# Performance work log

Measured on AMD Instinct MI355X. Metric: run time of the kernel, lower is better.

## Reference

```python
import jax, jax.numpy as jnp
import numpy as np

K = 7        # kernel_size (window)
PAD = 3      # padding = K // 2, stride = 1 -> spatial size preserved
G = 64       # groups
COUT = 64    # out_channels; d = COUT // G = 1 per-group channel dim
D = COUT // G


def _gconv(x, W):
    # grouped 1x1 conv: x [B, C, H, W], W [g, d_out_g, c_in_g] -> [B, g, d_out_g, H, W]
    B, C, H, Wd = x.shape
    g, d, c = W.shape
    return jnp.einsum('bgchw,gdc->bgdhw', x.reshape(B, g, c, H, Wd), W)


def _windows(x, k):
    # torch unfold(2,k,1).unfold(3,k,1) then flatten: row-major (i, j) window order
    # x [B, G, D, Hp, Wp] -> [B, G, D, H, W, k*k]
    Hp, Wp = x.shape[-2:]
    H, W = Hp - k + 1, Wp - k + 1
    return jnp.stack([x[..., i:i + H, j:j + W] for i in range(k) for j in range(k)], axis=-1)


def setup_inputs() -> dict:
    key = jax.random.key(0)
    ks = jax.random.split(key, 8)
    B, CIN, H, W = 4, 64, 56, 56
    RDIM = 256
    kaiming = np.sqrt(2.0 / COUT).astype(np.float32)  # fan_out for 1x1 conv
    x = jax.random.normal(ks[0], (B, CIN, H, W), jnp.float32)
    r = jax.random.normal(ks[1], (1, RDIM, K, K), jnp.float32)
    Wq = jax.random.normal(ks[2], (G, D, CIN // G), jnp.float32) * kaiming
    Wk = jax.random.normal(ks[3], (G, D, CIN // G), jnp.float32) * kaiming
    Wv = jax.random.normal(ks[4], (G, D, CIN // G), jnp.float32) * kaiming
    Wr = jax.random.normal(ks[5], (G, D, RDIM // G), jnp.float32) * kaiming
    u_p = jax.random.normal(ks[6], (1, G, D, 1, 1, 1), jnp.float32)
    v_p = jax.random.normal(ks[7], (1, G, D, 1, 1, 1), jnp.float32)
    return {'x': x, 'r': r, 'Wq': Wq, 'Wk': Wk, 'Wv': Wv, 'Wr': Wr, 'u_p': u_p, 'v_p': v_p}


def reference(x, r, Wq, Wk, Wv, Wr, u_p, v_p):
    B, _, H, W = x.shape
    xp = jnp.pad(x, ((0, 0), (0, 0), (PAD, PAD), (PAD, PAD)))
    q = _gconv(x, Wq)[..., None]              # [B,G,D,H,W,1]
    k_w = _windows(_gconv(xp, Wk), K)          # [B,G,D,H,W,K*K]
    v_w = _windows(_gconv(xp, Wv), K)          # [B,G,D,H,W,K*K]
    r_o = _gconv(r, Wr).reshape(1, G, D, 1, 1, K * K)
    # original: q*k + q*r + u*k + v*r == (q+u)*k + (q+v)*r
    # NOTE: original scale uses INTEGER division np.sqrt(groups // out_channels);
    # with groups == out_channels this is sqrt(1) = 1.0 (faithful).
    scale = float(np.sqrt(G // COUT))
    logits = ((q + u_p) * k_w + (q + v_p) * r_o).sum(axis=2, keepdims=True) * scale
    attn = jax.nn.softmax(logits, axis=-1)     # softmax over K*K window
    out = (attn * v_w).sum(axis=-1)            # [B,G,D,H,W]
    return out.reshape(B, -1, H, W)
```

## Files before the change

### kernel.cpp

```cpp
#include <hip/hip_runtime.h>
#include <hip/hip_bf16.h>

#define KW    7
#define PADW  3
#define HW    56
#define ROWS  8
#define TILE_H (ROWS + KW - 1)
#define TILE_W 64
#define NTHREADS 448
#define NCHUNK 7

#define LOG2E 1.44269504088896340736f

__global__ __launch_bounds__(NTHREADS) void saconv_kernel(
    const float* __restrict__ x,
    const float* __restrict__ r,
    const float* __restrict__ Wq,
    const float* __restrict__ Wk,
    const float* __restrict__ Wv,
    const float* __restrict__ Wr,
    const float* __restrict__ up,
    const float* __restrict__ vp,
    float* __restrict__ out)
{
    __shared__ float xs[TILE_H][TILE_W];
    __shared__ float ro[KW * KW];

    const int tid   = threadIdx.x;
    const int bid   = blockIdx.x;
    const int chunk = bid % NCHUNK;
    const int g     = (bid / NCHUNK) & 63;
    const int b     = bid / (NCHUNK * 64);
    const int y0    = chunk * ROWS;

    const float wq = Wq[g];
    const float wk = Wk[g];
    const float wv = Wv[g];
    const float ug = up[g];
    const float vg = vp[g];

    if (tid < KW * KW) {
        float acc = 0.f;
#pragma unroll
        for (int c = 0; c < 4; ++c) {
            acc += r[(g * 4 + c) * (KW * KW) + tid] * Wr[g * 4 + c];
        }
        ro[tid] = acc;
    }

    const float* xb = x + (size_t)(b * 64 + g) * (HW * HW);
    for (int idx = tid; idx < TILE_H * 62; idx += NTHREADS) {
        const int ty = idx / 62;
        const int tx = idx - ty * 62;
        const int gy = y0 - PADW + ty;
        const int gx = tx - PADW;
        float v = 0.f;
        if (gy >= 0 && gy < HW && gx >= 0 && gx < HW)
            v = xb[gy * HW + gx];
        xs[ty][tx] = v;
    }
    __syncthreads();

    const int row = tid / HW;
    const int col = tid - row * HW;

    const float xc  = xs[row + PADW][col + PADW];
    const float q   = xc * wq;
    const float a2  = (q + ug) * wk * LOG2E;
    const float cc2 = (q + vg) * LOG2E;

    float se = 0.f, sx = 0.f;
#pragma unroll
    for (int i = 0; i < KW; ++i) {
#pragma unroll
        for (int j = 0; j < KW; ++j) {
            const float xv = xs[row + i][col + j];
            const float l2 = __builtin_fmaf(a2, xv, cc2 * ro[i * KW + j]);
            const float e  = __builtin_amdgcn_exp2f(l2);
            se += e;
            sx = __builtin_fmaf(e, xv, sx);
        }
    }

    out[((size_t)(b * 64 + g) * HW + (y0 + row)) * HW + col] =
        wv * sx * __builtin_amdgcn_rcpf(se);
}

extern "C" void kernel_launch(void* const* d_in, const int* in_sizes, int n_in,
                              void* d_out, int out_size, void* d_ws, size_t ws_size,
                              hipStream_t stream) {
    const float* x  = (const float*)d_in[0];
    const float* r  = (const float*)d_in[1];
    const float* Wq = (const float*)d_in[2];
    const float* Wk = (const float*)d_in[3];
    const float* Wv = (const float*)d_in[4];
    const float* Wr = (const float*)d_in[5];
    const float* up = (const float*)d_in[6];
    const float* vp = (const float*)d_in[7];
    float* out = (float*)d_out;

    const int grid = 4 * 64 * NCHUNK;
    saconv_kernel<<<grid, NTHREADS, 0, stream>>>(x, r, Wq, Wk, Wv, Wr, up, vp, out);
}
```

Baseline: 76.43 us.

## Process two groups per block with float2 packed math and interleaved shared tile

Each block now handles a pair of groups. Shared memory holds an interleaved float2 tile and float2 relative logits, so the window loop can use packed FP32 ops (v_pk_fma/v_pk_mul) and 64-bit LDS reads. This halves the number of blocks, amortises the index math, and reduces LDS instructions per output. In exchange it doubles the LDS footprint per block and leaves fewer blocks to fill the GPU (896 vs 1792). The exp2 calls stay scalar.

```diff
diff --git a/kernel.cpp b/kernel.cpp
--- a/kernel.cpp
+++ b/kernel.cpp
@@ -12,6 +12,8 @@
 
 #define LOG2E 1.44269504088896340736f
 
+typedef float f2 __attribute__((ext_vector_type(2)));
+
 __global__ __launch_bounds__(NTHREADS) void saconv_kernel(
     const float* __restrict__ x,
     const float* __restrict__ r,
@@ -23,40 +25,47 @@
     const float* __restrict__ vp,
     float* __restrict__ out)
 {
-    __shared__ float xs[TILE_H][TILE_W];
-    __shared__ float ro[KW * KW];
+    __shared__ f2 xs[TILE_H][TILE_W];
+    __shared__ f2 ro2[KW * KW];
 
     const int tid   = threadIdx.x;
     const int bid   = blockIdx.x;
     const int chunk = bid % NCHUNK;
-    const int g     = (bid / NCHUNK) & 63;
-    const int b     = bid / (NCHUNK * 64);
+    const int gp    = (bid / NCHUNK) & 31;
+    const int b     = bid / (NCHUNK * 32);
     const int y0    = chunk * ROWS;
+    const int g0    = 2 * gp;
+    const int g1    = 2 * gp + 1;
 
-    const float wq = Wq[g];
-    const float wk = Wk[g];
-    const float wv = Wv[g];
-    const float ug = up[g];
-    const float vg = vp[g];
+    const f2 wq2 = {Wq[g0], Wq[g1]};
+    const f2 wk2 = {Wk[g0], Wk[g1]};
+    const f2 wv2 = {Wv[g0], Wv[g1]};
+    const f2 ug2 = {up[g0], up[g1]};
+    const f2 vg2 = {vp[g0], vp[g1]};
 
     if (tid < KW * KW) {
-        float acc = 0.f;
+        float a0 = 0.f, a1 = 0.f;
 #pragma unroll
         for (int c = 0; c < 4; ++c) {
-            acc += r[(g * 4 + c) * (KW * KW) + tid] * Wr[g * 4 + c];
+            a0 += r[(g0 * 4 + c) * (KW * KW) + tid] * Wr[g0 * 4 + c];
+            a1 += r[(g1 * 4 + c) * (KW * KW) + tid] * Wr[g1 * 4 + c];
         }
-        ro[tid] = acc;
+        f2 t; t.x = a0; t.y = a1;
+        ro2[tid] = t;
     }
 
-    const float* xb = x + (size_t)(b * 64 + g) * (HW * HW);
+    const float* xb0 = x + (size_t)(b * 64 + g0) * (HW * HW);
+    const float* xb1 = xb0 + HW * HW;
     for (int idx = tid; idx < TILE_H * 62; idx += NTHREADS) {
         const int ty = idx / 62;
         const int tx = idx - ty * 62;
         const int gy = y0 - PADW + ty;
         const int gx = tx - PADW;
-        float v = 0.f;
-        if (gy >= 0 && gy < HW && gx >= 0 && gx < HW)
-            v = xb[gy * HW + gx];
+        f2 v = {0.f, 0.f};
+        if (gy >= 0 && gy < HW && gx >= 0 && gx < HW) {
+            v.x = xb0[gy * HW + gx];
+            v.y = xb1[gy * HW + gx];
+        }
         xs[ty][tx] = v;
     }
     __syncthreads();
@@ -64,26 +73,33 @@
     const int row = tid / HW;
     const int col = tid - row * HW;
 
-    const float xc  = xs[row + PADW][col + PADW];
-    const float q   = xc * wq;
-    const float a2  = (q + ug) * wk * LOG2E;
-    const float cc2 = (q + vg) * LOG2E;
+    const f2 xc  = xs[row + PADW][col + PADW];
+    const f2 q   = xc * wq2;
+    const f2 a2  = (q + ug2) * wk2 * (f2){LOG2E, LOG2E};
+    const f2 cc2 = (q + vg2) * (f2){LOG2E, LOG2E};
 
-    float se = 0.f, sx = 0.f;
+    f2 se = {0.f, 0.f}, sx = {0.f, 0.f};
 #pragma unroll
     for (int i = 0; i < KW; ++i) {
 #pragma unroll
         for (int j = 0; j < KW; ++j) {
-            const float xv = xs[row + i][col + j];
-            const float l2 = __builtin_fmaf(a2, xv, cc2 * ro[i * KW + j]);
-            const float e  = __builtin_amdgcn_exp2f(l2);
+            const f2 xv = xs[row + i][col + j];
+            const f2 l2 = a2 * xv + cc2 * ro2[i * KW + j];
+            f2 e;
+            e.x = __builtin_amdgcn_exp2f(l2.x);
+            e.y = __builtin_amdgcn_exp2f(l2.y);
             se += e;
-            sx = __builtin_fmaf(e, xv, sx);
+            sx = e * xv + sx;
         }
     }
 
-    out[((size_t)(b * 64 + g) * HW + (y0 + row)) * HW + col] =
-        wv * sx * __builtin_amdgcn_rcpf(se);
+    f2 o;
+    o.x = wv2.x * sx.x * __builtin_amdgcn_rcpf(se.x);
+    o.y = wv2.y * sx.y * __builtin_amdgcn_rcpf(se.y);
+
+    const size_t base = ((size_t)(b * 64 + g0) * HW + (y0 + row)) * HW + col;
+    out[base] = o.x;
+    out[base + (size_t)HW * HW] = o.y;
 }
 
 extern "C" void kernel_launch(void* const* d_in, const int* in_sizes, int n_in,
@@ -99,6 +115,6 @@
     const float* vp = (const float*)d_in[7];
     float* out = (float*)d_out;
 
-    const int grid = 4 * 64 * NCHUNK;
+    const int grid = 4 * 32 * NCHUNK;
     saconv_kernel<<<grid, NTHREADS, 0, stream>>>(x, r, Wq, Wk, Wv, Wr, up, vp, out);
 }
```

New measurement: 77.27 us. Within noise of the previous version (+1.1%).

## Process full image plane per block with register-blocked 7 rows per thread

Applied to the files above, without the earlier changes.

Each block now handles one whole (batch, group) plane instead of an 8-row chunk, so the grid shrinks from 1792 to 256 blocks. Each thread computes 7 vertically adjacent outputs and reuses each loaded shared-memory row across all the outputs whose windows cover it. The relative-position table is held in registers. This cuts shared-memory loads and halo reloading, but uses more registers and gives fewer blocks than the 256 CUs, which may lower occupancy and latency hiding.

```diff
diff --git a/kernel.cpp b/kernel.cpp
--- a/kernel.cpp
+++ b/kernel.cpp
@@ -1,14 +1,13 @@
 #include <hip/hip_runtime.h>
 #include <hip/hip_bf16.h>
 
-#define KW    7
-#define PADW  3
-#define HW    56
-#define ROWS  8
-#define TILE_H (ROWS + KW - 1)
-#define TILE_W 64
+#define KW   7
+#define PADW 3
+#define HW   56
+#define PH   62
+#define LDW  64
 #define NTHREADS 448
-#define NCHUNK 7
+#define PPT  7
 
 #define LOG2E 1.44269504088896340736f
 
@@ -23,15 +22,13 @@
     const float* __restrict__ vp,
     float* __restrict__ out)
 {
-    __shared__ float xs[TILE_H][TILE_W];
+    __shared__ float xs[PH][LDW];
     __shared__ float ro[KW * KW];
 
-    const int tid   = threadIdx.x;
-    const int bid   = blockIdx.x;
-    const int chunk = bid % NCHUNK;
-    const int g     = (bid / NCHUNK) & 63;
-    const int b     = bid / (NCHUNK * 64);
-    const int y0    = chunk * ROWS;
+    const int tid = threadIdx.x;
+    const int bid = blockIdx.x;
+    const int g   = bid & 63;
+    const int b   = bid >> 6;
 
     const float wq = Wq[g];
     const float wk = Wk[g];
@@ -42,17 +39,16 @@
     if (tid < KW * KW) {
         float acc = 0.f;
 #pragma unroll
-        for (int c = 0; c < 4; ++c) {
+        for (int c = 0; c < 4; ++c)
             acc += r[(g * 4 + c) * (KW * KW) + tid] * Wr[g * 4 + c];
-        }
         ro[tid] = acc;
     }
 
     const float* xb = x + (size_t)(b * 64 + g) * (HW * HW);
-    for (int idx = tid; idx < TILE_H * 62; idx += NTHREADS) {
-        const int ty = idx / 62;
-        const int tx = idx - ty * 62;
-        const int gy = y0 - PADW + ty;
+    for (int idx = tid; idx < PH * LDW; idx += NTHREADS) {
+        const int ty = idx >> 6;
+        const int tx = idx & 63;
+        const int gy = ty - PADW;
         const int gx = tx - PADW;
         float v = 0.f;
         if (gy >= 0 && gy < HW && gx >= 0 && gx < HW)
@@ -61,29 +57,55 @@
     }
     __syncthreads();
 
-    const int row = tid / HW;
-    const int col = tid - row * HW;
+    const int col  = tid % HW;
+    const int rg   = tid / HW;
+    const int row0 = rg * PPT;
 
-    const float xc  = xs[row + PADW][col + PADW];
-    const float q   = xc * wq;
-    const float a2  = (q + ug) * wk * LOG2E;
-    const float cc2 = (q + vg) * LOG2E;
+    float rr[KW * KW];
+#pragma unroll
+    for (int k = 0; k < KW * KW; ++k) rr[k] = ro[k];
 
-    float se = 0.f, sx = 0.f;
+    float a2[PPT], cc2[PPT];
 #pragma unroll
-    for (int i = 0; i < KW; ++i) {
+    for (int p = 0; p < PPT; ++p) {
+        const float xc = xs[row0 + p + PADW][col + PADW];
+        const float q  = xc * wq;
+        a2[p]  = (q + ug) * wk * LOG2E;
+        cc2[p] = (q + vg) * LOG2E;
+    }
+
+    float se[PPT], sx[PPT];
 #pragma unroll
-        for (int j = 0; j < KW; ++j) {
-            const float xv = xs[row + i][col + j];
-            const float l2 = __builtin_fmaf(a2, xv, cc2 * ro[i * KW + j]);
-            const float e  = __builtin_amdgcn_exp2f(l2);
-            se += e;
-            sx = __builtin_fmaf(e, xv, sx);
+    for (int p = 0; p < PPT; ++p) { se[p] = 0.f; sx[p] = 0.f; }
+
+#pragma unroll
+    for (int R = 0; R < PPT + KW - 1; ++R) {
+        float xr[KW];
+#pragma unroll
+        for (int j = 0; j < KW; ++j)
+            xr[j] = xs[row0 + R][col + j];
+#pragma unroll
+        for (int p = 0; p < PPT; ++p) {
+            const int i = R - p;
+            if (i >= 0 && i < KW) {
+#pragma unroll
+                for (int j = 0; j < KW; ++j) {
+                    const float l2 = __builtin_fmaf(a2[p], xr[j],
+                                                    cc2[p] * rr[i * KW + j]);
+                    const float e  = __builtin_amdgcn_exp2f(l2);
+                    se[p] += e;
+                    sx[p] = __builtin_fmaf(e, xr[j], sx[p]);
+                }
+            }
         }
     }
 
-    out[((size_t)(b * 64 + g) * HW + (y0 + row)) * HW + col] =
-        wv * sx * __builtin_amdgcn_rcpf(se);
+    const size_t base = (size_t)(b * 64 + g) * (HW * HW);
+#pragma unroll
+    for (int p = 0; p < PPT; ++p) {
+        out[base + (row0 + p) * HW + col] =
+            wv * sx[p] * __builtin_amdgcn_rcpf(se[p]);
+    }
 }
 
 extern "C" void kernel_launch(void* const* d_in, const int* in_sizes, int n_in,
@@ -99,6 +121,6 @@
     const float* vp = (const float*)d_in[7];
     float* out = (float*)d_out;
 
-    const int grid = 4 * 64 * NCHUNK;
+    const int grid = 4 * 64;
     saconv_kernel<<<grid, NTHREADS, 0, stream>>>(x, r, Wq, Wk, Wv, Wr, up, vp, out);
 }
```

After: 127.5 us. +66.8%, slower.
